# Kernel tuning notes

Hardware: AMD Instinct MI355X
Metric: run time of the kernel (lower is better)

The kernel has to match this reference:

```python
import jax, jax.numpy as jnp
import numpy as np


def gcn_conv(x, src, dst, deg_inv_sqrt, W, b):
    # PyG GCNConv: h = x @ W, then symmetric-normalized scatter-add over edges
    # (edge list already includes self-loops; deg computed over it).
    h = x @ W                                   # [N, F_out]
    norm = deg_inv_sqrt[src] * deg_inv_sqrt[dst]  # [E]
    msgs = h[src] * norm[:, None]               # gather + scale
    out = jax.ops.segment_sum(msgs, dst, num_segments=x.shape[0])
    return out + b


def setup_inputs() -> dict:
    key = jax.random.key(0)
    k1, k2, k3, k4 = jax.random.split(key, 4)
    N, E, F_in, F_hid, F_out = 200000, 6400000, 128, 8, 16
    x = jax.random.normal(k1, (N, F_in), dtype=jnp.float32)
    edge_index = jax.random.randint(k2, (2, E), 0, N, dtype=jnp.int64)
    W1 = jax.random.normal(k3, (F_in, F_hid), dtype=jnp.float32) * (1.0 / np.sqrt(F_in))
    b1 = jnp.zeros((F_hid,), dtype=jnp.float32)
    W2 = jax.random.normal(k4, (F_hid, F_out), dtype=jnp.float32) * (1.0 / np.sqrt(F_hid))
    b2 = jnp.zeros((F_out,), dtype=jnp.float32)
    return {"x": x, "edge_index": edge_index, "W1": W1, "b1": b1, "W2": W2, "b2": b2}


def reference(x, edge_index, W1, b1, W2, b2):
    N = x.shape[0]
    # add self-loops (GCNConv default add_self_loops=True)
    loops = jnp.arange(N, dtype=edge_index.dtype)
    src = jnp.concatenate([edge_index[0], loops])
    dst = jnp.concatenate([edge_index[1], loops])
    deg = jax.ops.segment_sum(jnp.ones_like(dst, dtype=x.dtype), dst, num_segments=N)
    deg_inv_sqrt = jnp.where(deg > 0, jax.lax.rsqrt(deg), 0.0)
    h = jax.nn.relu(gcn_conv(x, src, dst, deg_inv_sqrt, W1, b1))
    # dropout is identity in eval mode (training=False)
    out = gcn_conv(h, src, dst, deg_inv_sqrt, W2, b2)
    return out
```

## Files before the change

### kernel.cpp

```cpp
#include <hip/hip_runtime.h>
#include <hip/hip_fp16.h>

#define F_IN  128
#define F_HID 8
#define F_OUT 16

#define SBSH  9
#define SBW   (1 << SBSH)
#define MAXB  400
#define BIN_CAP  32
#define FLUSH_G  16


typedef float f32x4 __attribute__((ext_vector_type(4)));

__global__ void init_gcur(int* __restrict__ gcur, int cap, int B) {
    int b = blockIdx.x * blockDim.x + threadIdx.x;
    if (b < B) gcur[b] = b * cap;
}

__global__ __launch_bounds__(512) void stage_bin(const int* __restrict__ ei,
                                                 int* __restrict__ gcur,
                                                 int* __restrict__ stage,
                                                 int E, int B, int per_block) {
    __shared__ int bin_cnt[MAXB];
    __shared__ int bin_buf[MAXB * BIN_CAP];
    for (int i = threadIdx.x; i < B; i += blockDim.x) bin_cnt[i] = 0;
    __syncthreads();
    const bool vec = ((E & 3) == 0);
    int base = blockIdx.x * per_block;
    int end  = min(E, base + per_block);
    for (int it = base; it < end; it += (int)blockDim.x * 4) {
        int e = it + (int)threadIdx.x * 4;
        int sv[4], dv[4], m4 = 0;
        if (vec && e + 3 < end) {
            int4 s4 = *(const int4*)(ei + e);
            int4 d4 = *(const int4*)(ei + E + e);
            sv[0] = s4.x; sv[1] = s4.y; sv[2] = s4.z; sv[3] = s4.w;
            dv[0] = d4.x; dv[1] = d4.y; dv[2] = d4.z; dv[3] = d4.w;
            m4 = 4;
        } else {
            for (int q = 0; e + q < end && q < 4; q++) { sv[q] = ei[e + q]; dv[q] = ei[E + e + q]; m4++; }
        }
        for (int q = 0; q < m4; q++) {
            int b   = dv[q] >> SBSH;
            int val = (sv[q] << SBSH) | (dv[q] & (SBW - 1));
            int pos = atomicAdd(&bin_cnt[b], 1);
            if (pos < BIN_CAP) {
                bin_buf[b * BIN_CAP + ((pos + b) & (BIN_CAP - 1))] = val;
            } else {
                int gp = atomicAdd(&gcur[b], 1);
                stage[gp] = val;
            }
        }
        __syncthreads();
        for (int b2 = threadIdx.x; b2 < B; b2 += blockDim.x) {
            int c = min(bin_cnt[b2], BIN_CAP);
            if (c >= FLUSH_G) {
                int m = c & ~(FLUSH_G - 1);
                int r = atomicAdd(&gcur[b2], m);
                for (int k = 0; k < m; k++)
                    stage[r + k] = bin_buf[b2 * BIN_CAP + ((k + b2) & (BIN_CAP - 1))];
                for (int k = m; k < c; k++)
                    bin_buf[b2 * BIN_CAP + ((k - m + b2) & (BIN_CAP - 1))] =
                        bin_buf[b2 * BIN_CAP + ((k + b2) & (BIN_CAP - 1))];
                bin_cnt[b2] = c - m;
            } else {
                bin_cnt[b2] = c;
            }
        }
        __syncthreads();
    }
    for (int b2 = threadIdx.x; b2 < B; b2 += blockDim.x) {
        int c = min(bin_cnt[b2], BIN_CAP);
        if (c > 0) {
            int r = atomicAdd(&gcur[b2], c);
            for (int k = 0; k < c; k++)
                stage[r + k] = bin_buf[b2 * BIN_CAP + ((k + b2) & (BIN_CAP - 1))];
        }
    }
}

__global__ __launch_bounds__(512) void scatter_csr(const int* __restrict__ stage,
                                                   const int* __restrict__ gcur,
                                                   int cap,
                                                   int* __restrict__ cnt,
                                                   float* __restrict__ dis,
                                                   int* __restrict__ row_start,
                                                   int* __restrict__ csr, int n) {
    __shared__ int s0[SBW], s1[SBW];
    int b  = blockIdx.x;
    int nb = b << SBSH;
    int i  = threadIdx.x;
    s0[i] = 0;
    __syncthreads();
    int base = b * cap;
    int num  = gcur[b] - base;
    for (int k = i; k < num; k += 512)
        atomicAdd(&s0[stage[base + k] & (SBW - 1)], 1);
    __syncthreads();
    int c = s0[i];
    if (nb + i < n) { cnt[nb + i] = c; dis[nb + i] = rsqrtf((float)(c + 1)); }
    int* src = s0; int* dst = s1;
    for (int off = 1; off < SBW; off <<= 1) {
        int v = src[i] + ((i >= off) ? src[i - off] : 0);
        dst[i] = v;
        __syncthreads();
        int* t = src; src = dst; dst = t;
    }
    int e = base + src[i] - c;
    if (nb + i < n) row_start[nb + i] = e;
    dst[i] = e;
    __syncthreads();
    for (int k = i; k < num; k += 512) {
        int v = stage[base + k];
        int pos = atomicAdd(&dst[v & (SBW - 1)], 1);
        csr[pos] = v >> SBSH;
    }
}

__global__ __launch_bounds__(256) void gemm1(const float* __restrict__ x,
                                             const float* __restrict__ W1,
                                             const float* __restrict__ dis,
                                             __half* __restrict__ g1, int n) {
    __shared__ float w2[F_HID * F_IN];
    for (int i = threadIdx.x; i < F_HID * F_IN; i += blockDim.x) {
        int f = i >> 7, k = i & (F_IN - 1);
        w2[i] = W1[k * F_HID + f];
    }
    __syncthreads();
    int t = blockIdx.x * blockDim.x + threadIdx.x;
    int node = t >> 3, l = t & 7;
    if (node >= n) return;
    const f32x4* xr = (const f32x4*)(x + (size_t)node * F_IN);
    float acc[F_HID];
#pragma unroll
    for (int f = 0; f < F_HID; f++) acc[f] = 0.0f;
#pragma unroll
    for (int it = 0; it < 4; it++) {
        int j = l + it * 8;
        f32x4 v = __builtin_nontemporal_load(xr + j);
#pragma unroll
        for (int f = 0; f < F_HID; f++) {
            const float* wf = &w2[f * F_IN + j * 4];
            acc[f] += v[0] * wf[0] + v[1] * wf[1] + v[2] * wf[2] + v[3] * wf[3];
        }
    }
#pragma unroll
    for (int f = 0; f < F_HID; f++) {
        acc[f] += __shfl_xor(acc[f], 1);
        acc[f] += __shfl_xor(acc[f], 2);
        acc[f] += __shfl_xor(acc[f], 4);
    }
    if (l == 0) {
        float d = dis[node];
        __half2 h[4];
#pragma unroll
        for (int p = 0; p < 4; p++) h[p] = __floats2half2_rn(acc[2 * p] * d, acc[2 * p + 1] * d);
        *(uint4*)(g1 + (size_t)node * F_HID) = *(uint4*)h;
    }
}

__global__ __launch_bounds__(256) void aggregate_relu(const int* __restrict__ csr,
                                                      const int* __restrict__ row_start,
                                                      const int* __restrict__ cnt,
                                                      const float* __restrict__ dis,
                                                      const float* __restrict__ b1,
                                                      const __half* __restrict__ gin,
                                                      __half* __restrict__ gout, int n) {
    __shared__ float bb[F_HID];
    if (threadIdx.x < F_HID) bb[threadIdx.x] = b1[threadIdx.x];
    __syncthreads();
    int t = blockIdx.x * blockDim.x + threadIdx.x;
    int node = t >> 3;
    int f = t & 7;
    if (node >= n) return;
    int beg = row_start[node];
    int c   = cnt[node];
    float acc = __half2float(gin[(size_t)node * F_HID + f]);
    int j = 0;
    int cm8 = c & ~7;
    for (; j < cm8; j += 8) {
        int vv = __builtin_nontemporal_load(csr + beg + j + f);
        int s0 = __shfl(vv, 0, 8), s1 = __shfl(vv, 1, 8);
        int s2 = __shfl(vv, 2, 8), s3 = __shfl(vv, 3, 8);
        int s4 = __shfl(vv, 4, 8), s5 = __shfl(vv, 5, 8);
        int s6 = __shfl(vv, 6, 8), s7 = __shfl(vv, 7, 8);
        float a0 = __half2float(gin[(size_t)s0 * F_HID + f]);
        float a1 = __half2float(gin[(size_t)s1 * F_HID + f]);
        float a2 = __half2float(gin[(size_t)s2 * F_HID + f]);
        float a3 = __half2float(gin[(size_t)s3 * F_HID + f]);
        float a4 = __half2float(gin[(size_t)s4 * F_HID + f]);
        float a5 = __half2float(gin[(size_t)s5 * F_HID + f]);
        float a6 = __half2float(gin[(size_t)s6 * F_HID + f]);
        float a7 = __half2float(gin[(size_t)s7 * F_HID + f]);
        acc += ((a0 + a1) + (a2 + a3)) + ((a4 + a5) + (a6 + a7));
    }
    for (; j < c; j++) {
        int s = __builtin_nontemporal_load(csr + beg + j);
        acc += __half2float(gin[(size_t)s * F_HID + f]);
    }
    float d = dis[node];
    float r = fmaxf(acc * d + bb[f], 0.0f) * d;
    gout[(size_t)node * F_HID + f] = __float2half(r);
}

__global__ __launch_bounds__(256) void aggregate_out(const int* __restrict__ csr,
                                                     const int* __restrict__ row_start,
                                                     const int* __restrict__ cnt,
                                                     const float* __restrict__ dis,
                                                     const float* __restrict__ W2,
                                                     const float* __restrict__ b2,
                                                     const __half* __restrict__ gin,
                                                     float* __restrict__ out, int n) {
    __shared__ float w[F_HID * F_OUT];
    __shared__ float bb[F_OUT];
    if (threadIdx.x < F_HID * F_OUT) w[threadIdx.x] = W2[threadIdx.x];
    if (threadIdx.x < F_OUT) bb[threadIdx.x] = b2[threadIdx.x];
    __syncthreads();
    int t = blockIdx.x * blockDim.x + threadIdx.x;
    int node = t >> 3;
    int f = t & 7;
    if (node >= n) return;
    int beg = row_start[node];
    int c   = cnt[node];
    float acc = __half2float(gin[(size_t)node * F_HID + f]);
    int j = 0;
    int cm8 = c & ~7;
    for (; j < cm8; j += 8) {
        int vv = __builtin_nontemporal_load(csr + beg + j + f);
        int s0 = __shfl(vv, 0, 8), s1 = __shfl(vv, 1, 8);
        int s2 = __shfl(vv, 2, 8), s3 = __shfl(vv, 3, 8);
        int s4 = __shfl(vv, 4, 8), s5 = __shfl(vv, 5, 8);
        int s6 = __shfl(vv, 6, 8), s7 = __shfl(vv, 7, 8);
        float a0 = __half2float(gin[(size_t)s0 * F_HID + f]);
        float a1 = __half2float(gin[(size_t)s1 * F_HID + f]);
        float a2 = __half2float(gin[(size_t)s2 * F_HID + f]);
        float a3 = __half2float(gin[(size_t)s3 * F_HID + f]);
        float a4 = __half2float(gin[(size_t)s4 * F_HID + f]);
        float a5 = __half2float(gin[(size_t)s5 * F_HID + f]);
        float a6 = __half2float(gin[(size_t)s6 * F_HID + f]);
        float a7 = __half2float(gin[(size_t)s7 * F_HID + f]);
        acc += ((a0 + a1) + (a2 + a3)) + ((a4 + a5) + (a6 + a7));
    }
    for (; j < c; j++) {
        int s = __builtin_nontemporal_load(csr + beg + j);
        acc += __half2float(gin[(size_t)s * F_HID + f]);
    }
    float a_self = acc * dis[node];
    float o0 = bb[2 * f], o1 = bb[2 * f + 1];
#pragma unroll
    for (int k = 0; k < 8; k++) {
        float ak = __shfl(a_self, k, 8);
        o0 += ak * w[k * F_OUT + 2 * f];
        o1 += ak * w[k * F_OUT + 2 * f + 1];
    }
    *(float2*)(out + (size_t)node * F_OUT + 2 * f) = make_float2(o0, o1);
}

extern "C" void kernel_launch(void* const* d_in, const int* in_sizes, int n_in,
                              void* d_out, int out_size, void* d_ws, size_t ws_size,
                              hipStream_t stream) {
    const float* x  = (const float*)d_in[0];
    const int*   ei = (const int*)d_in[1];
    const float* W1 = (const float*)d_in[2];
    const float* b1 = (const float*)d_in[3];
    const float* W2 = (const float*)d_in[4];
    const float* b2 = (const float*)d_in[5];
    float* out = (float*)d_out;

    const int N = in_sizes[0] / F_IN;
    const int E = in_sizes[1] / 2;
    const int B = (N + SBW - 1) >> SBSH;

    int avg = (E + B - 1) / B;
    int cap = (avg + avg / 16 + 255) & ~255;

    int*    stage     = (int*)d_ws;
    int*    csr       = stage + (size_t)B * cap;
    float*  dis       = (float*)(csr + (size_t)B * cap);
    __half* gA        = (__half*)(dis + N);
    __half* gB        = (__half*)((int*)gA + (size_t)N * 4);
    int*    cnt       = (int*)gB + (size_t)N * 4;
    int*    row_start = cnt + N;
    int*    gcur      = row_start + N;

    const int BT = 256;
    dim3 thr(BT);
    dim3 blkA(((size_t)N * F_HID + BT - 1) / BT);

    int per_block = ((E + 639) / 640 + 2047) & ~2047;
    int SBLK = (E + per_block - 1) / per_block;

    init_gcur     <<<dim3((B + BT - 1) / BT), thr, 0, stream>>>(gcur, cap, B);
    stage_bin     <<<dim3(SBLK), dim3(512), 0, stream>>>(ei, gcur, stage, E, B, per_block);
    scatter_csr   <<<dim3(B),   dim3(512), 0, stream>>>(stage, gcur, cap, cnt, dis, row_start, csr, N);
    gemm1         <<<blkA, thr, 0, stream>>>(x, W1, dis, gA, N);
    aggregate_relu<<<blkA, thr, 0, stream>>>(csr, row_start, cnt, dis, b1, gA, gB, N);
    aggregate_out <<<blkA, thr, 0, stream>>>(csr, row_start, cnt, dis, W2, b2, gB, out, N);
}
```

Measured before the change: 440.7 us.

## Gather half2 pairs with 4 lanes per node and widen CSR scatter blocks

Both aggregation kernels now use 4 lanes per node, and each lane gathers one __half2 (two features) instead of one half. This halves the number of gather instructions and threads per edge. The final W2 projection now reads float4 weights directly from global memory instead of staging them in LDS. scatter_csr is launched with 1024 threads per bucket, and threads beyond the 512 bins only help with the histogram and scatter loops. The changes add shuffle and guard logic and increase LDS atomic contention per block.

```diff
diff --git a/kernel.cpp b/kernel.cpp
--- a/kernel.cpp
+++ b/kernel.cpp
@@ -81,38 +81,39 @@
     }
 }
 
-__global__ __launch_bounds__(512) void scatter_csr(const int* __restrict__ stage,
-                                                   const int* __restrict__ gcur,
-                                                   int cap,
-                                                   int* __restrict__ cnt,
-                                                   float* __restrict__ dis,
-                                                   int* __restrict__ row_start,
-                                                   int* __restrict__ csr, int n) {
+__global__ __launch_bounds__(1024) void scatter_csr(const int* __restrict__ stage,
+                                                    const int* __restrict__ gcur,
+                                                    int cap,
+                                                    int* __restrict__ cnt,
+                                                    float* __restrict__ dis,
+                                                    int* __restrict__ row_start,
+                                                    int* __restrict__ csr, int n) {
     __shared__ int s0[SBW], s1[SBW];
     int b  = blockIdx.x;
     int nb = b << SBSH;
     int i  = threadIdx.x;
-    s0[i] = 0;
+    if (i < SBW) s0[i] = 0;
     __syncthreads();
     int base = b * cap;
     int num  = gcur[b] - base;
-    for (int k = i; k < num; k += 512)
+    for (int k = i; k < num; k += 1024)
         atomicAdd(&s0[stage[base + k] & (SBW - 1)], 1);
     __syncthreads();
-    int c = s0[i];
-    if (nb + i < n) { cnt[nb + i] = c; dis[nb + i] = rsqrtf((float)(c + 1)); }
+    int c = (i < SBW) ? s0[i] : 0;
+    if (i < SBW && nb + i < n) { cnt[nb + i] = c; dis[nb + i] = rsqrtf((float)(c + 1)); }
     int* src = s0; int* dst = s1;
     for (int off = 1; off < SBW; off <<= 1) {
-        int v = src[i] + ((i >= off) ? src[i - off] : 0);
-        dst[i] = v;
+        if (i < SBW) dst[i] = src[i] + ((i >= off) ? src[i - off] : 0);
         __syncthreads();
         int* t = src; src = dst; dst = t;
     }
-    int e = base + src[i] - c;
-    if (nb + i < n) row_start[nb + i] = e;
-    dst[i] = e;
-    __syncthreads();
-    for (int k = i; k < num; k += 512) {
+    if (i < SBW) {
+        int e = base + src[i] - c;
+        if (nb + i < n) row_start[nb + i] = e;
+        dst[i] = e;
+    }
+    __syncthreads();
+    for (int k = i; k < num; k += 1024) {
         int v = stage[base + k];
         int pos = atomicAdd(&dst[v & (SBW - 1)], 1);
         csr[pos] = v >> SBSH;
@@ -168,41 +169,48 @@
                                                       const float* __restrict__ b1,
                                                       const __half* __restrict__ gin,
                                                       __half* __restrict__ gout, int n) {
-    __shared__ float bb[F_HID];
-    if (threadIdx.x < F_HID) bb[threadIdx.x] = b1[threadIdx.x];
-    __syncthreads();
     int t = blockIdx.x * blockDim.x + threadIdx.x;
-    int node = t >> 3;
-    int f = t & 7;
+    int node = t >> 2;
+    int l = t & 3;
     if (node >= n) return;
+    const __half2* g2 = (const __half2*)gin;
     int beg = row_start[node];
     int c   = cnt[node];
-    float acc = __half2float(gin[(size_t)node * F_HID + f]);
+    float2 acc = __half22float2(g2[(unsigned)node * 4 + l]);
     int j = 0;
     int cm8 = c & ~7;
     for (; j < cm8; j += 8) {
-        int vv = __builtin_nontemporal_load(csr + beg + j + f);
-        int s0 = __shfl(vv, 0, 8), s1 = __shfl(vv, 1, 8);
-        int s2 = __shfl(vv, 2, 8), s3 = __shfl(vv, 3, 8);
-        int s4 = __shfl(vv, 4, 8), s5 = __shfl(vv, 5, 8);
-        int s6 = __shfl(vv, 6, 8), s7 = __shfl(vv, 7, 8);
-        float a0 = __half2float(gin[(size_t)s0 * F_HID + f]);
-        float a1 = __half2float(gin[(size_t)s1 * F_HID + f]);
-        float a2 = __half2float(gin[(size_t)s2 * F_HID + f]);
-        float a3 = __half2float(gin[(size_t)s3 * F_HID + f]);
-        float a4 = __half2float(gin[(size_t)s4 * F_HID + f]);
-        float a5 = __half2float(gin[(size_t)s5 * F_HID + f]);
-        float a6 = __half2float(gin[(size_t)s6 * F_HID + f]);
-        float a7 = __half2float(gin[(size_t)s7 * F_HID + f]);
-        acc += ((a0 + a1) + (a2 + a3)) + ((a4 + a5) + (a6 + a7));
+        int va = __builtin_nontemporal_load(csr + beg + j + l);
+        int vb = __builtin_nontemporal_load(csr + beg + j + 4 + l);
+        int s0 = __shfl(va, 0, 4), s1 = __shfl(va, 1, 4);
+        int s2 = __shfl(va, 2, 4), s3 = __shfl(va, 3, 4);
+        int s4 = __shfl(vb, 0, 4), s5 = __shfl(vb, 1, 4);
+        int s6 = __shfl(vb, 2, 4), s7 = __shfl(vb, 3, 4);
+        __half2 h0 = g2[(unsigned)s0 * 4 + l];
+        __half2 h1 = g2[(unsigned)s1 * 4 + l];
+        __half2 h2 = g2[(unsigned)s2 * 4 + l];
+        __half2 h3 = g2[(unsigned)s3 * 4 + l];
+        __half2 h4 = g2[(unsigned)s4 * 4 + l];
+        __half2 h5 = g2[(unsigned)s5 * 4 + l];
+        __half2 h6 = g2[(unsigned)s6 * 4 + l];
+        __half2 h7 = g2[(unsigned)s7 * 4 + l];
+        float2 f0 = __half22float2(h0), f1 = __half22float2(h1);
+        float2 f2 = __half22float2(h2), f3 = __half22float2(h3);
+        float2 f4 = __half22float2(h4), f5 = __half22float2(h5);
+        float2 f6 = __half22float2(h6), f7 = __half22float2(h7);
+        acc.x += ((f0.x + f1.x) + (f2.x + f3.x)) + ((f4.x + f5.x) + (f6.x + f7.x));
+        acc.y += ((f0.y + f1.y) + (f2.y + f3.y)) + ((f4.y + f5.y) + (f6.y + f7.y));
     }
     for (; j < c; j++) {
         int s = __builtin_nontemporal_load(csr + beg + j);
-        acc += __half2float(gin[(size_t)s * F_HID + f]);
+        float2 a = __half22float2(g2[(unsigned)s * 4 + l]);
+        acc.x += a.x; acc.y += a.y;
     }
     float d = dis[node];
-    float r = fmaxf(acc * d + bb[f], 0.0f) * d;
-    gout[(size_t)node * F_HID + f] = __float2half(r);
+    float2 bv = *(const float2*)(b1 + 2 * l);
+    float rx = fmaxf(fmaf(acc.x, d, bv.x), 0.0f) * d;
+    float ry = fmaxf(fmaf(acc.y, d, bv.y), 0.0f) * d;
+    ((__half2*)gout)[(unsigned)node * 4 + l] = __floats2half2_rn(rx, ry);
 }
 
 __global__ __launch_bounds__(256) void aggregate_out(const int* __restrict__ csr,
@@ -213,49 +221,58 @@
                                                      const float* __restrict__ b2,
                                                      const __half* __restrict__ gin,
                                                      float* __restrict__ out, int n) {
-    __shared__ float w[F_HID * F_OUT];
-    __shared__ float bb[F_OUT];
-    if (threadIdx.x < F_HID * F_OUT) w[threadIdx.x] = W2[threadIdx.x];
-    if (threadIdx.x < F_OUT) bb[threadIdx.x] = b2[threadIdx.x];
-    __syncthreads();
     int t = blockIdx.x * blockDim.x + threadIdx.x;
-    int node = t >> 3;
-    int f = t & 7;
+    int node = t >> 2;
+    int l = t & 3;
     if (node >= n) return;
+    const __half2* g2 = (const __half2*)gin;
     int beg = row_start[node];
     int c   = cnt[node];
-    float acc = __half2float(gin[(size_t)node * F_HID + f]);
+    float2 acc = __half22float2(g2[(unsigned)node * 4 + l]);
     int j = 0;
     int cm8 = c & ~7;
     for (; j < cm8; j += 8) {
-        int vv = __builtin_nontemporal_load(csr + beg + j + f);
-        int s0 = __shfl(vv, 0, 8), s1 = __shfl(vv, 1, 8);
-        int s2 = __shfl(vv, 2, 8), s3 = __shfl(vv, 3, 8);
-        int s4 = __shfl(vv, 4, 8), s5 = __shfl(vv, 5, 8);
-        int s6 = __shfl(vv, 6, 8), s7 = __shfl(vv, 7, 8);
-        float a0 = __half2float(gin[(size_t)s0 * F_HID + f]);
-        float a1 = __half2float(gin[(size_t)s1 * F_HID + f]);
-        float a2 = __half2float(gin[(size_t)s2 * F_HID + f]);
-        float a3 = __half2float(gin[(size_t)s3 * F_HID + f]);
-        float a4 = __half2float(gin[(size_t)s4 * F_HID + f]);
-        float a5 = __half2float(gin[(size_t)s5 * F_HID + f]);
-        float a6 = __half2float(gin[(size_t)s6 * F_HID + f]);
-        float a7 = __half2float(gin[(size_t)s7 * F_HID + f]);
-        acc += ((a0 + a1) + (a2 + a3)) + ((a4 + a5) + (a6 + a7));
+        int va = __builtin_nontemporal_load(csr + beg + j + l);
+        int vb = __builtin_nontemporal_load(csr + beg + j + 4 + l);
+        int s0 = __shfl(va, 0, 4), s1 = __shfl(va, 1, 4);
+        int s2 = __shfl(va, 2, 4), s3 = __shfl(va, 3, 4);
+        int s4 = __shfl(vb, 0, 4), s5 = __shfl(vb, 1, 4);
+        int s6 = __shfl(vb, 2, 4), s7 = __shfl(vb, 3, 4);
+        __half2 h0 = g2[(unsigned)s0 * 4 + l];
+        __half2 h1 = g2[(unsigned)s1 * 4 + l];
+        __half2 h2 = g2[(unsigned)s2 * 4 + l];
+        __half2 h3 = g2[(unsigned)s3 * 4 + l];
+        __half2 h4 = g2[(unsigned)s4 * 4 + l];
+        __half2 h5 = g2[(unsigned)s5 * 4 + l];
+        __half2 h6 = g2[(unsigned)s6 * 4 + l];
+        __half2 h7 = g2[(unsigned)s7 * 4 + l];
+        float2 f0 = __half22float2(h0), f1 = __half22float2(h1);
+        float2 f2 = __half22float2(h2), f3 = __half22float2(h3);
+        float2 f4 = __half22float2(h4), f5 = __half22float2(h5);
+        float2 f6 = __half22float2(h6), f7 = __half22float2(h7);
+        acc.x += ((f0.x + f1.x) + (f2.x + f3.x)) + ((f4.x + f5.x) + (f6.x + f7.x));
+        acc.y += ((f0.y + f1.y) + (f2.y + f3.y)) + ((f4.y + f5.y) + (f6.y + f7.y));
     }
     for (; j < c; j++) {
         int s = __builtin_nontemporal_load(csr + beg + j);
-        acc += __half2float(gin[(size_t)s * F_HID + f]);
-    }
-    float a_self = acc * dis[node];
-    float o0 = bb[2 * f], o1 = bb[2 * f + 1];
-#pragma unroll
-    for (int k = 0; k < 8; k++) {
-        float ak = __shfl(a_self, k, 8);
-        o0 += ak * w[k * F_OUT + 2 * f];
-        o1 += ak * w[k * F_OUT + 2 * f + 1];
-    }
-    *(float2*)(out + (size_t)node * F_OUT + 2 * f) = make_float2(o0, o1);
+        float2 a = __half22float2(g2[(unsigned)s * 4 + l]);
+        acc.x += a.x; acc.y += a.y;
+    }
+    float d = dis[node];
+    float ax = acc.x * d, ay = acc.y * d;
+    float4 o = ((const float4*)b2)[l];
+#pragma unroll
+    for (int s = 0; s < 4; s++) {
+        float axs = __shfl(ax, s, 4);
+        float ays = __shfl(ay, s, 4);
+        float4 w0 = ((const float4*)W2)[(2 * s) * 4 + l];
+        float4 w1 = ((const float4*)W2)[(2 * s + 1) * 4 + l];
+        o.x = fmaf(axs, w0.x, fmaf(ays, w1.x, o.x));
+        o.y = fmaf(axs, w0.y, fmaf(ays, w1.y, o.y));
+        o.z = fmaf(axs, w0.z, fmaf(ays, w1.z, o.z));
+        o.w = fmaf(axs, w0.w, fmaf(ays, w1.w, o.w));
+    }
+    *(float4*)(out + (size_t)node * F_OUT + 4 * l) = o;
 }
 
 extern "C" void kernel_launch(void* const* d_in, const int* in_sizes, int n_in,
@@ -287,15 +304,16 @@
 
     const int BT = 256;
     dim3 thr(BT);
-    dim3 blkA(((size_t)N * F_HID + BT - 1) / BT);
+    dim3 blkG(((size_t)N * 8 + BT - 1) / BT);
+    dim3 blkA(((size_t)N * 4 + BT - 1) / BT);
 
     int per_block = ((E + 639) / 640 + 2047) & ~2047;
     int SBLK = (E + per_block - 1) / per_block;
 
     init_gcur     <<<dim3((B + BT - 1) / BT), thr, 0, stream>>>(gcur, cap, B);
     stage_bin     <<<dim3(SBLK), dim3(512), 0, stream>>>(ei, gcur, stage, E, B, per_block);
-    scatter_csr   <<<dim3(B),   dim3(512), 0, stream>>>(stage, gcur, cap, cnt, dis, row_start, csr, N);
-    gemm1         <<<blkA, thr, 0, stream>>>(x, W1, dis, gA, N);
+    scatter_csr   <<<dim3(B),   dim3(1024), 0, stream>>>(stage, gcur, cap, cnt, dis, row_start, csr, N);
+    gemm1         <<<blkG, thr, 0, stream>>>(x, W1, dis, gA, N);
     aggregate_relu<<<blkA, thr, 0, stream>>>(csr, row_start, cnt, dis, b1, gA, gB, N);
     aggregate_out <<<blkA, thr, 0, stream>>>(csr, row_start, cnt, dis, W2, b2, gB, out, N);
 }
```

Result: no change. 434.5 us, median of 2 (-1.4%).
